# Kernel optimization log

Measured on AMD Instinct MI355X. Metric: run time of the kernel, lower is better.

The kernel has to match this reference:

```python
import jax, jax.numpy as jnp
import numpy as np

B, S, D_IN, E, H = 4, 2048, 768, 768, 12
HD = E // H                      # 64
WIN_PCT = 10                     # window_size init arg (percent of valid length)
MAX_LEN = 2048
MIN_WIN = 2
PAD = -1e9
TEMP = 1.0


def setup_inputs() -> dict:
    key = jax.random.key(0)
    k1, k2, k3 = jax.random.split(key, 3)
    return {
        "x": jax.random.normal(k1, (B, S, D_IN), dtype=jnp.float32),
        "src_key_padding_mask": jnp.zeros((B, S), dtype=jnp.int32),   # 0 = valid token
        "matrix_mask": jnp.zeros((B, S, S), dtype=jnp.float32),       # additive mask, 0 or PAD
        "qkv_w": jax.random.normal(k2, (3 * E, D_IN), dtype=jnp.float32) * 0.02,
        "qkv_b": jnp.zeros((3 * E,), dtype=jnp.float32),
        "o_w": jax.random.normal(k3, (E, E), dtype=jnp.float32) * 0.02,
        "o_b": jnp.zeros((E,), dtype=jnp.float32),
    }


def _sliding_window_mask(src_key_padding_mask, matrix_mask):
    # per-sample window size = ceil(valid_len * WIN_PCT / 100), clamped to >= MIN_WIN
    lens = (src_key_padding_mask == 0).sum(axis=1)                    # [B]
    clipped = jnp.minimum(lens, MAX_LEN).astype(jnp.float32)
    wsz = jnp.maximum(jnp.ceil(clipped * WIN_PCT / 100.0), MIN_WIN)   # [B] float ok for compare
    idx = jnp.arange(S)
    dist = jnp.abs(idx[None, :, None] - idx[None, None, :])           # [1,S,S]
    window_mask = dist > wsz[:, None, None]                           # [B,S,S] bool
    merged = window_mask | (matrix_mask == PAD)
    return jnp.where(merged, PAD, matrix_mask)                        # [B,S,S]


def reference(x, src_key_padding_mask, matrix_mask, qkv_w, qkv_b, o_w, o_b):
    mask = _sliding_window_mask(src_key_padding_mask, matrix_mask)    # [B,S,S]
    qkv = x @ qkv_w.T + qkv_b                                         # [B,S,3E]
    # torch: reshape(B,S,H,3*HD) then chunk along last dim
    qkv = qkv.reshape(B, S, H, 3 * HD).transpose(0, 2, 1, 3)          # [B,H,S,3*HD]
    q, k, v = jnp.split(qkv, 3, axis=-1)                              # each [B,H,S,HD]
    scale = 1.0 / np.sqrt(HD)
    logits = jnp.einsum("bhqd,bhkd->bhqk", q, k) * scale + mask[:, None]
    attn = jax.nn.softmax(logits / TEMP, axis=-1)                     # [B,H,S,S]
    values = jnp.einsum("bhqk,bhkd->bhqd", attn, v)                   # [B,H,S,HD]
    attn_mean = attn.mean(axis=1)                                     # [B,S,S]
    values = values.transpose(0, 2, 1, 3).reshape(B, S, E)            # [B,S,E]
    o = values @ o_w.T + o_b
    return (o, attn_mean)
```

## Files before the change

kernel.cpp:

```cpp
#include <hip/hip_runtime.h>

#define SEQ 2048
#define NB 4
#define DIN 768
#define EDIM 768
#define NH 12
#define QKVN 2304
#define QKW 1536
#define SCALE 0.125f
#define PADV -1e9f
#define INV12 (0.0833333333f)
#define PSW 520

typedef unsigned short ushort_t;
typedef __attribute__((ext_vector_type(8))) short bf16x8;
typedef __attribute__((ext_vector_type(4))) float f32x4;

__device__ __forceinline__ float bf2f(ushort_t u) {
    union { unsigned int i; float f; } v; v.i = ((unsigned int)u) << 16; return v.f;
}
__device__ __forceinline__ ushort_t f2bf(float f) {
    union { float f; unsigned int i; } v; v.f = f;
    unsigned int r = (v.i + 0x7fffu + ((v.i >> 16) & 1u)) >> 16;
    return (ushort_t)r;
}
__device__ __forceinline__ void gl_lds16(const ushort_t* g, ushort_t* l) {
    __builtin_amdgcn_global_load_lds(
        (const __attribute__((address_space(1))) unsigned int*)(g),
        (__attribute__((address_space(3))) unsigned int*)(l),
        16, 0, 0);
}

__global__ void wsz_kernel(const int* __restrict__ mask, int* __restrict__ wszp) {
    int b = blockIdx.x;
    __shared__ int cnt;
    if (threadIdx.x == 0) cnt = 0;
    __syncthreads();
    int local = 0;
    for (int s = threadIdx.x; s < SEQ; s += blockDim.x)
        local += (mask[b * SEQ + s] == 0) ? 1 : 0;
    for (int o = 32; o; o >>= 1) local += __shfl_down(local, o, 64);
    if ((threadIdx.x & 63) == 0) atomicAdd(&cnt, local);
    __syncthreads();
    if (threadIdx.x == 0) {
        int len = cnt; if (len > 2048) len = 2048;
        float w = ceilf(((float)len * 10.0f) / 100.0f);
        int wsz = (int)w;
        if (wsz < 2) wsz = 2;
        wszp[b] = wsz;
    }
}

__global__ void cvt3_kernel(const float* __restrict__ s0, int n0,
                            const float* __restrict__ s1, int n1,
                            const float* __restrict__ s2, int n2,
                            ushort_t* __restrict__ d0, ushort_t* __restrict__ d1,
                            ushort_t* __restrict__ d2) {
    int i = blockIdx.x * blockDim.x + threadIdx.x;
    const float* src; ushort_t* dst; int off;
    if (i < n0)               { src = s0; dst = d0; off = i; }
    else if (i < n0 + n1)     { src = s1; dst = d1; off = i - n0; }
    else if (i < n0 + n1 + n2){ src = s2; dst = d2; off = i - n0 - n1; }
    else return;
    float4 f = ((const float4*)src)[off];
    ushort4 u;
    u.x = f2bf(f.x); u.y = f2bf(f.y); u.z = f2bf(f.z); u.w = f2bf(f.w);
    ((ushort4*)dst)[off] = u;
}

__global__ void flag_kernel(const float* __restrict__ mmask, const int* __restrict__ wszp,
                            int* __restrict__ flags) {
    const int b = blockIdx.z, i16 = blockIdx.y;
    const int wsz = wszp[b];
    const int i0 = i16 * 16;
    const int jt0 = max(0, i0 - wsz) >> 6;
    const int jt1 = min(SEQ - 1, i0 + 15 + wsz) >> 6;
    const int jt = jt0 + blockIdx.x;
    if (jt > jt1) return;
    int any = 0;
    for (int e = threadIdx.x; e < 1024; e += 256) {
        int row = e >> 6, col = e & 63;
        float v = mmask[((size_t)b * SEQ + i0 + row) * SEQ + jt * 64 + col];
        any |= (v != 0.f);
    }
    if (any) flags[(b * 128 + i16) * 32 + jt] = 1;
}

template<int MODE>
__global__ __launch_bounds__(256) void mfma_gemm128(
    const ushort_t* __restrict__ A, const ushort_t* __restrict__ Bw,
    const float* __restrict__ bias, float* __restrict__ outf,
    ushort_t* __restrict__ qk, ushort_t* __restrict__ vt, int N, int K)
{
    __shared__ __align__(16) ushort_t Al[128 * 64];
    __shared__ __align__(16) ushort_t Bl[128 * 64];
    const int tid  = threadIdx.x;
    const int w    = tid >> 6;
    const int l    = tid & 63;
    const int quad = l >> 4;
    const int lr   = l & 15;
    const int mw   = (w >> 1) * 64;
    const int nw   = (w & 1) * 64;
    const int bm   = blockIdx.y * 128;
    const int bn   = blockIdx.x * 128;
    const int srow = l >> 3;
    const int sg   = (l & 7) ^ srow;

    f32x4 acc[4][4];
    #pragma unroll
    for (int i = 0; i < 4; ++i)
        #pragma unroll
        for (int j = 0; j < 4; ++j)
            #pragma unroll
            for (int r = 0; r < 4; ++r) acc[i][j][r] = 0.f;

    const ushort_t* ga = A  + (size_t)(bm + w * 32 + srow) * K + sg * 8;
    const ushort_t* gb = Bw + (size_t)(bn + w * 32 + srow) * K + sg * 8;
    ushort_t* la = &Al[(w * 32) * 64];
    ushort_t* lb = &Bl[(w * 32) * 64];

    for (int k0 = 0; k0 < K; k0 += 64) {
        __syncthreads();
        #pragma unroll
        for (int i = 0; i < 4; ++i)
            gl_lds16(ga + (size_t)(i * 8) * K + k0, la + i * 8 * 64);
        #pragma unroll
        for (int i = 0; i < 4; ++i)
            gl_lds16(gb + (size_t)(i * 8) * K + k0, lb + i * 8 * 64);
        __syncthreads();
        #pragma unroll
        for (int s = 0; s < 2; ++s) {
            bf16x8 af[4], bf[4];
            #pragma unroll
            for (int t = 0; t < 4; ++t)
                af[t] = *(const bf16x8*)&Al[(mw + t * 16 + lr) * 64 + (((4 * s + quad) ^ (lr & 7)) * 8)];
            #pragma unroll
            for (int t = 0; t < 4; ++t)
                bf[t] = *(const bf16x8*)&Bl[(nw + t * 16 + lr) * 64 + (((4 * s + quad) ^ (lr & 7)) * 8)];
            #pragma unroll
            for (int mt = 0; mt < 4; ++mt)
                #pragma unroll
                for (int nt = 0; nt < 4; ++nt)
                    acc[mt][nt] = __builtin_amdgcn_mfma_f32_16x16x32_bf16(af[mt], bf[nt], acc[mt][nt], 0, 0, 0);
        }
    }

    #pragma unroll
    for (int nt = 0; nt < 4; ++nt) {
        const int gn = bn + nw + nt * 16 + lr;
        const float bv = bias[gn];
        const int hh  = gn / 192;
        const int rem = gn - hh * 192;
        #pragma unroll
        for (int mt = 0; mt < 4; ++mt) {
            const int gm0 = bm + mw + mt * 16 + quad * 4;
            if (MODE == 0) {
                #pragma unroll
                for (int r = 0; r < 4; ++r)
                    outf[(size_t)(gm0 + r) * N + gn] = acc[mt][nt][r] + bv;
            } else if (rem < 128) {
                #pragma unroll
                for (int r = 0; r < 4; ++r)
                    qk[(size_t)(gm0 + r) * QKW + hh * 128 + rem] = f2bf(acc[mt][nt][r] + bv);
            } else {
                const int bb  = gm0 >> 11;
                const int tok = gm0 & (SEQ - 1);
                ushort4 st;
                st.x = f2bf(acc[mt][nt][0] + bv);
                st.y = f2bf(acc[mt][nt][1] + bv);
                st.z = f2bf(acc[mt][nt][2] + bv);
                st.w = f2bf(acc[mt][nt][3] + bv);
                *(ushort4*)&vt[((size_t)(bb * NH + hh) * 64 + (rem - 128)) * SEQ + tok] = st;
            }
        }
    }
}

__global__ __launch_bounds__(768) void attn_kernel(
    const ushort_t* __restrict__ qk,
    const ushort_t* __restrict__ vt,
    const float* __restrict__ mmask,
    const int* __restrict__ wszp,
    const int* __restrict__ flags,
    ushort_t* __restrict__ values,
    float* __restrict__ attn_out)
{
    __shared__ __align__(16) ushort_t Ps[3][16 * PSW];
    __shared__ float lsump[3][4][16];
    const int tid  = threadIdx.x;
    const int w    = tid >> 6;
    const int hg   = w >> 2;
    const int ww   = w & 3;
    const int lane = tid & 63;
    const int quad = lane >> 4;
    const int lr   = lane & 15;

    const int lin  = blockIdx.x;
    const int s    = lin & 1;
    const int b    = (lin >> 1) & 3;
    const int i16  = (lin >> 3) + 64 * s;
    const int iq0  = i16 * 16;

    const int wsz  = wszp[b];
    const int jlo  = max(0, iq0 - wsz);
    const int jhi  = min(SEQ - 1, iq0 + 15 + wsz);
    const int jt0  = jlo >> 6;
    const int nch  = (jhi >> 6) - jt0 + 1;
    const int jbase = jt0 << 6;
    const int span  = nch << 6;
    const int fbase = (b * 128 + i16) * 32;

    const int arow = tid & 15;
    const int acg  = tid >> 4;
    float acc[16];
    #pragma unroll
    for (int k = 0; k < 16; ++k) acc[k] = 0.f;

    const ushort_t* kbase = qk + (size_t)b * SEQ * QKW + 64;
    const ushort_t* vhead = vt + (size_t)b * NH * 64 * SEQ;

    for (int hp = 0; hp < NH / 3; ++hp) {
        const int h  = hp * 3 + hg;
        const int hq = h * 128;
        const ushort_t* qbase = qk + (size_t)(b * SEQ + iq0 + lr) * QKW + hq;
        const bf16x8 qf0 = *(const bf16x8*)(qbase + quad * 8);
        const bf16x8 qf1 = *(const bf16x8*)(qbase + 32 + quad * 8);

        float ls[4] = {0.f, 0.f, 0.f, 0.f};
        #pragma unroll
        for (int cc = 0; cc < 2; ++cc) {
            const int ci = ww + cc * 4;
            if (ci < nch) {
                const int jc = jbase + ci * 64;
                f32x4 s4[4];
                #pragma unroll
                for (int t = 0; t < 4; ++t) {
                    const ushort_t* kr = kbase + (size_t)(jc + t * 16 + lr) * QKW + hq;
                    bf16x8 kf0 = *(const bf16x8*)(kr + quad * 8);
                    bf16x8 kf1 = *(const bf16x8*)(kr + 32 + quad * 8);
                    #pragma unroll
                    for (int r = 0; r < 4; ++r) s4[t][r] = 0.f;
                    s4[t] = __builtin_amdgcn_mfma_f32_16x16x32_bf16(qf0, kf0, s4[t], 0, 0, 0);
                    s4[t] = __builtin_amdgcn_mfma_f32_16x16x32_bf16(qf1, kf1, s4[t], 0, 0, 0);
                }
                const int anym = flags[fbase + jt0 + ci];
                #pragma unroll
                for (int t = 0; t < 4; ++t) {
                    const int gj = jc + t * 16 + lr;
                    #pragma unroll
                    for (int r = 0; r < 4; ++r) {
                        const int gi = iq0 + quad * 4 + r;
                        float mm = 0.f;
                        if (anym) mm = mmask[((size_t)b * SEQ + gi) * SEQ + gj];
                        const int dist = gi > gj ? gi - gj : gj - gi;
                        const float p = (dist > wsz) ? 0.f : __expf(fmaf(s4[t][r], SCALE, mm));
                        ls[r] += p;
                        Ps[hg][(quad * 4 + r) * PSW + (ci * 64 + t * 16 + lr)] = f2bf(p);
                    }
                }
            }
        }
        #pragma unroll
        for (int r = 0; r < 4; ++r) {
            #pragma unroll
            for (int m = 8; m; m >>= 1) ls[r] += __shfl_xor(ls[r], m, 16);
        }
        if (lr == 0) {
            #pragma unroll
            for (int r = 0; r < 4; ++r) lsump[hg][ww][quad * 4 + r] = ls[r];
        }
        __syncthreads();

        if (acg < 32 && acg * 16 < span) {
            const float l0 = lsump[0][0][arow] + lsump[0][1][arow] + lsump[0][2][arow] + lsump[0][3][arow];
            const float l1 = lsump[1][0][arow] + lsump[1][1][arow] + lsump[1][2][arow] + lsump[1][3][arow];
            const float l2 = lsump[2][0][arow] + lsump[2][1][arow] + lsump[2][2][arow] + lsump[2][3][arow];
            const float sc0 = INV12 / l0;
            const float sc1 = INV12 / l1;
            const float sc2 = INV12 / l2;
            const ushort_t* p0 = &Ps[0][arow * PSW + acg * 16];
            const ushort_t* p1 = &Ps[1][arow * PSW + acg * 16];
            const ushort_t* p2 = &Ps[2][arow * PSW + acg * 16];
            #pragma unroll
            for (int k = 0; k < 4; ++k) {
                ushort4 u0 = *(const ushort4*)(p0 + k * 4);
                ushort4 u1 = *(const ushort4*)(p1 + k * 4);
                ushort4 u2 = *(const ushort4*)(p2 + k * 4);
                acc[k * 4 + 0] += bf2f(u0.x) * sc0 + bf2f(u1.x) * sc1 + bf2f(u2.x) * sc2;
                acc[k * 4 + 1] += bf2f(u0.y) * sc0 + bf2f(u1.y) * sc1 + bf2f(u2.y) * sc2;
                acc[k * 4 + 2] += bf2f(u0.z) * sc0 + bf2f(u1.z) * sc1 + bf2f(u2.z) * sc2;
                acc[k * 4 + 3] += bf2f(u0.w) * sc0 + bf2f(u1.w) * sc1 + bf2f(u2.w) * sc2;
            }
        }

        {
            f32x4 oacc;
            #pragma unroll
            for (int r = 0; r < 4; ++r) oacc[r] = 0.f;
            const ushort_t* vrow = vhead + (size_t)(h * 64 + ww * 16 + lr) * SEQ + jbase;
            for (int ci = 0; ci < nch; ++ci) {
                const int tok0 = ci * 64;
                #pragma unroll
                for (int s2 = 0; s2 < 2; ++s2) {
                    bf16x8 pa = *(const bf16x8*)&Ps[hg][lr * PSW + tok0 + s2 * 32 + quad * 8];
                    bf16x8 vf = *(const bf16x8*)(vrow + tok0 + s2 * 32 + quad * 8);
                    oacc = __builtin_amdgcn_mfma_f32_16x16x32_bf16(pa, vf, oacc, 0, 0, 0);
                }
            }
            float lr4[4];
            #pragma unroll
            for (int r = 0; r < 4; ++r)
                lr4[r] = lsump[hg][0][quad * 4 + r] + lsump[hg][1][quad * 4 + r] +
                         lsump[hg][2][quad * 4 + r] + lsump[hg][3][quad * 4 + r];
            #pragma unroll
            for (int r = 0; r < 4; ++r) {
                const int row = iq0 + quad * 4 + r;
                values[(size_t)(b * SEQ + row) * EDIM + h * 64 + ww * 16 + lr] =
                    f2bf(oacc[r] / lr4[r]);
            }
        }
        __syncthreads();
    }

    if (acg < 32 && acg * 16 < span) {
        float* dst = attn_out + ((size_t)b * SEQ + iq0 + arow) * SEQ + jbase + acg * 16;
        #pragma unroll
        for (int k = 0; k < 4; ++k) {
            float4 v = { acc[k * 4 + 0], acc[k * 4 + 1], acc[k * 4 + 2], acc[k * 4 + 3] };
            *(float4*)(dst + k * 4) = v;
        }
    }
    {
        const int c4lo = jbase >> 2;
        const int c4hi = (jbase + span) >> 2;
        const float4 z = {0.f, 0.f, 0.f, 0.f};
        for (int f = tid; f < 16 * 512; f += 768) {
            const int i  = f >> 9;
            const int c4 = f & 511;
            if (c4 < c4lo || c4 >= c4hi)
                *(float4*)(attn_out + ((size_t)b * SEQ + iq0 + i) * SEQ + c4 * 4) = z;
        }
    }
}

extern "C" void kernel_launch(void* const* d_in, const int* in_sizes, int n_in,
                              void* d_out, int out_size, void* d_ws, size_t ws_size,
                              hipStream_t stream) {
    const float* x      = (const float*)d_in[0];
    const int*   pad    = (const int*)d_in[1];
    const float* mmask  = (const float*)d_in[2];
    const float* qkv_w  = (const float*)d_in[3];
    const float* qkv_b  = (const float*)d_in[4];
    const float* o_w    = (const float*)d_in[5];
    const float* o_b    = (const float*)d_in[6];

    float* out_o    = (float*)d_out;
    float* out_attn = out_o + (size_t)NB * SEQ * EDIM;

    ushort_t* qk     = (ushort_t*)d_ws;
    ushort_t* vt     = qk + (size_t)NB * SEQ * QKW;
    ushort_t* xb     = vt + (size_t)NB * NH * 64 * SEQ;
    ushort_t* values = xb;
    ushort_t* wqkvb  = xb + (size_t)NB * SEQ * DIN;
    ushort_t* wob    = wqkvb + (size_t)QKVN * DIN;
    int*      wszp   = (int*)(wob + (size_t)EDIM * EDIM);
    int*      flags  = wszp + 4;

    hipMemsetAsync(flags, 0, (size_t)NB * 128 * 32 * sizeof(int), stream);

    wsz_kernel<<<NB, 256, 0, stream>>>(pad, wszp);
    flag_kernel<<<dim3(8, 128, NB), 256, 0, stream>>>(mmask, wszp, flags);

    const int nx = NB * SEQ * DIN / 4, nw1 = QKVN * DIN / 4, nw2 = EDIM * EDIM / 4;
    cvt3_kernel<<<(nx + nw1 + nw2 + 255) / 256, 256, 0, stream>>>(
        x, nx, qkv_w, nw1, o_w, nw2, xb, wqkvb, wob);

    mfma_gemm128<1><<<dim3(QKVN / 128, (NB * SEQ) / 128), 256, 0, stream>>>(
        xb, wqkvb, qkv_b, nullptr, qk, vt, QKVN, DIN);

    attn_kernel<<<512, 768, 0, stream>>>(
        qk, vt, mmask, wszp, flags, values, out_attn);

    mfma_gemm128<0><<<dim3(EDIM / 128, (NB * SEQ) / 128), 256, 0, stream>>>(
        values, wob, o_b, out_o, nullptr, nullptr, EDIM, EDIM);
}
```

Baseline: 344.4 us.

## Assign one head per wave and accumulate attention mean via LDS atomics

Restructures the attention kernel so each of the 12 waves owns one head for a 16-query tile. It replaces the per-head-group loop with its block-wide barriers by a two-pass softmax: one pass for row sums, then a recompute pass that does P·V with MFMA. The head-averaged attention map is built with LDS float atomics into a shared accumulator and written out in a single coalesced pass that also emits the zeros. The cost is QK^T computed twice, many LDS atomics, and changed occupancy hints.

```diff
diff --git a/kernel.cpp b/kernel.cpp
--- a/kernel.cpp
+++ b/kernel.cpp
@@ -10,7 +10,7 @@
 #define SCALE 0.125f
 #define PADV -1e9f
 #define INV12 (0.0833333333f)
-#define PSW 520
+#define ACCW 523
 
 typedef unsigned short ushort_t;
 typedef __attribute__((ext_vector_type(8))) short bf16x8;
@@ -23,6 +23,9 @@
     union { float f; unsigned int i; } v; v.f = f;
     unsigned int r = (v.i + 0x7fffu + ((v.i >> 16) & 1u)) >> 16;
     return (ushort_t)r;
+}
+__device__ __forceinline__ unsigned int pack2bf(float a, float b) {
+    return (unsigned int)f2bf(a) | ((unsigned int)f2bf(b) << 16);
 }
 __device__ __forceinline__ void gl_lds16(const ushort_t* g, ushort_t* l) {
     __builtin_amdgcn_global_load_lds(
@@ -176,7 +179,7 @@
     }
 }
 
-__global__ __launch_bounds__(768) void attn_kernel(
+__global__ __launch_bounds__(768, 6) void attn_kernel(
     const ushort_t* __restrict__ qk,
     const ushort_t* __restrict__ vt,
     const float* __restrict__ mmask,
@@ -185,15 +188,13 @@
     ushort_t* __restrict__ values,
     float* __restrict__ attn_out)
 {
-    __shared__ __align__(16) ushort_t Ps[3][16 * PSW];
-    __shared__ float lsump[3][4][16];
+    __shared__ float accs[16 * ACCW];
+    __shared__ __align__(16) ushort_t Pbuf[12 * 16 * 72];
     const int tid  = threadIdx.x;
     const int w    = tid >> 6;
-    const int hg   = w >> 2;
-    const int ww   = w & 3;
     const int lane = tid & 63;
     const int quad = lane >> 4;
-    const int lr   = lane & 15;
+    const int l15  = lane & 15;
 
     const int lin  = blockIdx.x;
     const int s    = lin & 1;
@@ -210,136 +211,124 @@
     const int span  = nch << 6;
     const int fbase = (b * 128 + i16) * 32;
 
-    const int arow = tid & 15;
-    const int acg  = tid >> 4;
-    float acc[16];
+    for (int i = tid; i < 16 * ACCW; i += 768) accs[i] = 0.f;
+    __syncthreads();
+
+    const int h = w;
+    const ushort_t* qbase = qk + (size_t)(b * SEQ + iq0 + l15) * QKW + h * 128;
+    const bf16x8 qf0 = *(const bf16x8*)(qbase + quad * 8);
+    const bf16x8 qf1 = *(const bf16x8*)(qbase + 32 + quad * 8);
+    const ushort_t* kbase = qk + (size_t)b * SEQ * QKW + h * 128 + 64;
+    const ushort_t* vbase = vt + (size_t)((b * NH + h) * 64) * SEQ;
+
+    const int gi = iq0 + l15;
+    const float* mrow = mmask + ((size_t)b * SEQ + gi) * SEQ;
+
+    float lsum = 0.f;
+    for (int ci = 0; ci < nch; ++ci) {
+        const int jc = jbase + ci * 64;
+        const int anym = flags[fbase + jt0 + ci];
+        #pragma unroll
+        for (int t = 0; t < 4; ++t) {
+            const ushort_t* kr = kbase + (size_t)(jc + t * 16 + l15) * QKW;
+            bf16x8 kf0 = *(const bf16x8*)(kr + quad * 8);
+            bf16x8 kf1 = *(const bf16x8*)(kr + 32 + quad * 8);
+            f32x4 s4;
+            #pragma unroll
+            for (int r = 0; r < 4; ++r) s4[r] = 0.f;
+            s4 = __builtin_amdgcn_mfma_f32_16x16x32_bf16(kf0, qf0, s4, 0, 0, 0);
+            s4 = __builtin_amdgcn_mfma_f32_16x16x32_bf16(kf1, qf1, s4, 0, 0, 0);
+            #pragma unroll
+            for (int r = 0; r < 4; ++r) {
+                const int gj = jc + t * 16 + quad * 4 + r;
+                float mm = 0.f;
+                if (anym) mm = mrow[gj];
+                const int dist = gi > gj ? gi - gj : gj - gi;
+                const float p = (dist > wsz) ? 0.f : __expf(fmaf(s4[r], SCALE, mm));
+                lsum += p;
+            }
+        }
+    }
+    lsum += __shfl_xor(lsum, 16);
+    lsum += __shfl_xor(lsum, 32);
+    const float invl = 1.0f / lsum;
+    const float sc   = invl * INV12;
+
+    f32x4 oacc[4];
     #pragma unroll
-    for (int k = 0; k < 16; ++k) acc[k] = 0.f;
-
-    const ushort_t* kbase = qk + (size_t)b * SEQ * QKW + 64;
-    const ushort_t* vhead = vt + (size_t)b * NH * 64 * SEQ;
-
-    for (int hp = 0; hp < NH / 3; ++hp) {
-        const int h  = hp * 3 + hg;
-        const int hq = h * 128;
-        const ushort_t* qbase = qk + (size_t)(b * SEQ + iq0 + lr) * QKW + hq;
-        const bf16x8 qf0 = *(const bf16x8*)(qbase + quad * 8);
-        const bf16x8 qf1 = *(const bf16x8*)(qbase + 32 + quad * 8);
-
-        float ls[4] = {0.f, 0.f, 0.f, 0.f};
-        #pragma unroll
-        for (int cc = 0; cc < 2; ++cc) {
-            const int ci = ww + cc * 4;
-            if (ci < nch) {
-                const int jc = jbase + ci * 64;
-                f32x4 s4[4];
-                #pragma unroll
-                for (int t = 0; t < 4; ++t) {
-                    const ushort_t* kr = kbase + (size_t)(jc + t * 16 + lr) * QKW + hq;
-                    bf16x8 kf0 = *(const bf16x8*)(kr + quad * 8);
-                    bf16x8 kf1 = *(const bf16x8*)(kr + 32 + quad * 8);
-                    #pragma unroll
-                    for (int r = 0; r < 4; ++r) s4[t][r] = 0.f;
-                    s4[t] = __builtin_amdgcn_mfma_f32_16x16x32_bf16(qf0, kf0, s4[t], 0, 0, 0);
-                    s4[t] = __builtin_amdgcn_mfma_f32_16x16x32_bf16(qf1, kf1, s4[t], 0, 0, 0);
-                }
-                const int anym = flags[fbase + jt0 + ci];
-                #pragma unroll
-                for (int t = 0; t < 4; ++t) {
-                    const int gj = jc + t * 16 + lr;
-                    #pragma unroll
-                    for (int r = 0; r < 4; ++r) {
-                        const int gi = iq0 + quad * 4 + r;
-                        float mm = 0.f;
-                        if (anym) mm = mmask[((size_t)b * SEQ + gi) * SEQ + gj];
-                        const int dist = gi > gj ? gi - gj : gj - gi;
-                        const float p = (dist > wsz) ? 0.f : __expf(fmaf(s4[t][r], SCALE, mm));
-                        ls[r] += p;
-                        Ps[hg][(quad * 4 + r) * PSW + (ci * 64 + t * 16 + lr)] = f2bf(p);
-                    }
-                }
-            }
-        }
-        #pragma unroll
-        for (int r = 0; r < 4; ++r) {
-            #pragma unroll
-            for (int m = 8; m; m >>= 1) ls[r] += __shfl_xor(ls[r], m, 16);
-        }
-        if (lr == 0) {
-            #pragma unroll
-            for (int r = 0; r < 4; ++r) lsump[hg][ww][quad * 4 + r] = ls[r];
-        }
-        __syncthreads();
-
-        if (acg < 32 && acg * 16 < span) {
-            const float l0 = lsump[0][0][arow] + lsump[0][1][arow] + lsump[0][2][arow] + lsump[0][3][arow];
-            const float l1 = lsump[1][0][arow] + lsump[1][1][arow] + lsump[1][2][arow] + lsump[1][3][arow];
-            const float l2 = lsump[2][0][arow] + lsump[2][1][arow] + lsump[2][2][arow] + lsump[2][3][arow];
-            const float sc0 = INV12 / l0;
-            const float sc1 = INV12 / l1;
-            const float sc2 = INV12 / l2;
-            const ushort_t* p0 = &Ps[0][arow * PSW + acg * 16];
-            const ushort_t* p1 = &Ps[1][arow * PSW + acg * 16];
-            const ushort_t* p2 = &Ps[2][arow * PSW + acg * 16];
-            #pragma unroll
-            for (int k = 0; k < 4; ++k) {
-                ushort4 u0 = *(const ushort4*)(p0 + k * 4);
-                ushort4 u1 = *(const ushort4*)(p1 + k * 4);
-                ushort4 u2 = *(const ushort4*)(p2 + k * 4);
-                acc[k * 4 + 0] += bf2f(u0.x) * sc0 + bf2f(u1.x) * sc1 + bf2f(u2.x) * sc2;
-                acc[k * 4 + 1] += bf2f(u0.y) * sc0 + bf2f(u1.y) * sc1 + bf2f(u2.y) * sc2;
-                acc[k * 4 + 2] += bf2f(u0.z) * sc0 + bf2f(u1.z) * sc1 + bf2f(u2.z) * sc2;
-                acc[k * 4 + 3] += bf2f(u0.w) * sc0 + bf2f(u1.w) * sc1 + bf2f(u2.w) * sc2;
-            }
-        }
-
-        {
-            f32x4 oacc;
-            #pragma unroll
-            for (int r = 0; r < 4; ++r) oacc[r] = 0.f;
-            const ushort_t* vrow = vhead + (size_t)(h * 64 + ww * 16 + lr) * SEQ + jbase;
-            for (int ci = 0; ci < nch; ++ci) {
-                const int tok0 = ci * 64;
-                #pragma unroll
-                for (int s2 = 0; s2 < 2; ++s2) {
-                    bf16x8 pa = *(const bf16x8*)&Ps[hg][lr * PSW + tok0 + s2 * 32 + quad * 8];
-                    bf16x8 vf = *(const bf16x8*)(vrow + tok0 + s2 * 32 + quad * 8);
-                    oacc = __builtin_amdgcn_mfma_f32_16x16x32_bf16(pa, vf, oacc, 0, 0, 0);
-                }
-            }
-            float lr4[4];
-            #pragma unroll
-            for (int r = 0; r < 4; ++r)
-                lr4[r] = lsump[hg][0][quad * 4 + r] + lsump[hg][1][quad * 4 + r] +
-                         lsump[hg][2][quad * 4 + r] + lsump[hg][3][quad * 4 + r];
+    for (int t = 0; t < 4; ++t)
+        #pragma unroll
+        for (int r = 0; r < 4; ++r) oacc[t][r] = 0.f;
+
+    ushort_t* prow = &Pbuf[(w * 16 + l15) * 72];
+
+    for (int ci = 0; ci < nch; ++ci) {
+        const int jc = jbase + ci * 64;
+        const int anym = flags[fbase + jt0 + ci];
+        #pragma unroll
+        for (int t = 0; t < 4; ++t) {
+            const ushort_t* kr = kbase + (size_t)(jc + t * 16 + l15) * QKW;
+            bf16x8 kf0 = *(const bf16x8*)(kr + quad * 8);
+            bf16x8 kf1 = *(const bf16x8*)(kr + 32 + quad * 8);
+            f32x4 s4;
+            #pragma unroll
+            for (int r = 0; r < 4; ++r) s4[r] = 0.f;
+            s4 = __builtin_amdgcn_mfma_f32_16x16x32_bf16(kf0, qf0, s4, 0, 0, 0);
+            s4 = __builtin_amdgcn_mfma_f32_16x16x32_bf16(kf1, qf1, s4, 0, 0, 0);
+            float p[4];
             #pragma unroll
             for (int r = 0; r < 4; ++r) {
-                const int row = iq0 + quad * 4 + r;
-                values[(size_t)(b * SEQ + row) * EDIM + h * 64 + ww * 16 + lr] =
-                    f2bf(oacc[r] / lr4[r]);
-            }
-        }
-        __syncthreads();
-    }
-
-    if (acg < 32 && acg * 16 < span) {
-        float* dst = attn_out + ((size_t)b * SEQ + iq0 + arow) * SEQ + jbase + acg * 16;
-        #pragma unroll
-        for (int k = 0; k < 4; ++k) {
-            float4 v = { acc[k * 4 + 0], acc[k * 4 + 1], acc[k * 4 + 2], acc[k * 4 + 3] };
-            *(float4*)(dst + k * 4) = v;
-        }
-    }
+                const int gj = jc + t * 16 + quad * 4 + r;
+                float mm = 0.f;
+                if (anym) mm = mrow[gj];
+                const int dist = gi > gj ? gi - gj : gj - gi;
+                p[r] = (dist > wsz) ? 0.f : __expf(fmaf(s4[r], SCALE, mm));
+                if (p[r] != 0.f)
+                    atomicAdd(&accs[l15 * ACCW + (jc - jbase) + t * 16 + quad * 4 + r], p[r] * sc);
+            }
+            uint2 pk;
+            pk.x = pack2bf(p[0], p[1]);
+            pk.y = pack2bf(p[2], p[3]);
+            *(uint2*)(prow + t * 16 + quad * 4) = pk;
+        }
+        #pragma unroll
+        for (int g = 0; g < 2; ++g) {
+            bf16x8 pa = *(const bf16x8*)(prow + g * 32 + quad * 8);
+            #pragma unroll
+            for (int t2 = 0; t2 < 4; ++t2) {
+                bf16x8 vf = *(const bf16x8*)(vbase + (size_t)(t2 * 16 + l15) * SEQ + jc + g * 32 + quad * 8);
+                oacc[t2] = __builtin_amdgcn_mfma_f32_16x16x32_bf16(pa, vf, oacc[t2], 0, 0, 0);
+            }
+        }
+    }
+
     {
-        const int c4lo = jbase >> 2;
-        const int c4hi = (jbase + span) >> 2;
-        const float4 z = {0.f, 0.f, 0.f, 0.f};
-        for (int f = tid; f < 16 * 512; f += 768) {
-            const int i  = f >> 9;
-            const int c4 = f & 511;
-            if (c4 < c4lo || c4 >= c4hi)
-                *(float4*)(attn_out + ((size_t)b * SEQ + iq0 + i) * SEQ + c4 * 4) = z;
-        }
+        float invr[4];
+        #pragma unroll
+        for (int r = 0; r < 4; ++r) invr[r] = __shfl(invl, quad * 4 + r, 16);
+        #pragma unroll
+        for (int t2 = 0; t2 < 4; ++t2) {
+            #pragma unroll
+            for (int r = 0; r < 4; ++r) {
+                values[(size_t)(b * SEQ + iq0 + quad * 4 + r) * EDIM + h * 64 + t2 * 16 + l15] =
+                    f2bf(oacc[t2][r] * invr[r]);
+            }
+        }
+    }
+    __syncthreads();
+
+    for (int f = tid; f < 16 * 512; f += 768) {
+        const int i  = f >> 9;
+        const int j  = (f & 511) * 4;
+        const int o  = j - jbase;
+        float4 v = {0.f, 0.f, 0.f, 0.f};
+        if (o >= 0 && o < span) {
+            v.x = accs[i * ACCW + o + 0];
+            v.y = accs[i * ACCW + o + 1];
+            v.z = accs[i * ACCW + o + 2];
+            v.w = accs[i * ACCW + o + 3];
+        }
+        *(float4*)(attn_out + ((size_t)b * SEQ + iq0 + i) * SEQ + j) = v;
     }
 }
 
```

After: 502.8 us. 46.0% more time.
